# Kernel optimization log

Hardware: AMD Instinct MI355X
Metric: run time of the kernel (lower is better)

The kernel has to match this reference:

```python
import jax, jax.numpy as jnp
import numpy as np

N_NODES = 50000
N_EDGES = 800000
N_GRAPHS = 128
D_IN = 128
D_HID = 128
D_OUT = 3


def setup_inputs() -> dict:
    key = jax.random.key(0)
    ks = jax.random.split(key, 8)

    def lin_w(k, fan_in, fan_out):
        return (jax.random.normal(k, (fan_in, fan_out), jnp.float32)
                * (1.0 / np.sqrt(fan_in)))

    return {
        "x": jax.random.normal(ks[0], (N_NODES, D_IN), jnp.float32),
        "edge_index": jax.random.randint(ks[1], (2, N_EDGES), 0, N_NODES),
        "batch": jnp.sort(jax.random.randint(ks[2], (N_NODES,), 0, N_GRAPHS)),
        "W1": lin_w(ks[3], D_IN, D_HID),  "b1": jnp.zeros((D_HID,), jnp.float32),
        "W2": lin_w(ks[4], D_HID, D_HID), "b2": jnp.zeros((D_HID,), jnp.float32),
        "W3": lin_w(ks[5], D_HID, D_HID), "b3": jnp.zeros((D_HID,), jnp.float32),
        "Wlin": lin_w(ks[6], D_HID, D_OUT), "blin": jnp.zeros((D_OUT,), jnp.float32),
    }


def reference(x, edge_index, batch, W1, b1, W2, b2, W3, b3, Wlin, blin):
    n = x.shape[0]
    # PyG GCNConv: add self-loops, symmetric normalization D^-1/2 A D^-1/2
    loop = jnp.arange(n)
    row = jnp.concatenate([edge_index[0], loop])  # source nodes [E+N]
    col = jnp.concatenate([edge_index[1], loop])  # target nodes [E+N]
    deg = jax.ops.segment_sum(jnp.ones_like(col, dtype=x.dtype), col,
                              num_segments=n)
    dinv = jnp.where(deg > 0, jax.lax.rsqrt(deg), 0.0)
    norm = dinv[row] * dinv[col]  # [E+N]

    def gcn_conv(h, W, b):
        hw = h @ W                              # [N, D] linear (no bias)
        msg = hw[row] * norm[:, None]           # gather + scale [E+N, D]
        return jax.ops.segment_sum(msg, col, num_segments=n) + b

    h = jax.nn.relu(gcn_conv(x, W1, b1))
    h = jax.nn.relu(gcn_conv(h, W2, b2))
    h = gcn_conv(h, W3, b3)

    # global mean pool over graphs (dropout is identity in eval mode)
    sums = jax.ops.segment_sum(h, batch, num_segments=N_GRAPHS)
    counts = jax.ops.segment_sum(jnp.ones((n,), h.dtype), batch,
                                 num_segments=N_GRAPHS)
    pooled = sums / jnp.maximum(counts, 1.0)[:, None]
    return pooled @ Wlin + blin
```

## Files before the change

### kernel.cpp

```cpp
#include <hip/hip_runtime.h>

#define N_NODES 50000
#define N_EDGES 800000
#define N_GRAPHS 128
#define D 128
#define NCHUNK 196

__device__ __forceinline__ void fma4(float4& a, float w, const float4& h) {
    a.x += w * h.x; a.y += w * h.y; a.z += w * h.z; a.w += w * h.w;
}
__device__ __forceinline__ void add4(float4& a, const float4& h) {
    a.x += h.x; a.y += h.y; a.z += h.z; a.w += h.w;
}

__global__ __launch_bounds__(256) void k_count(const int* __restrict__ col,
                                               int* __restrict__ counts) {
    int e = blockIdx.x * 256 + threadIdx.x;
    if (e < N_EDGES) atomicAdd(&counts[col[e]], 1);
}

__global__ __launch_bounds__(256) void k_dinv(const int* __restrict__ counts,
                                              float* __restrict__ dinv) {
    int i = blockIdx.x * 256 + threadIdx.x;
    if (i < N_NODES) dinv[i] = rsqrtf((float)(counts[i] + 1));
}

__global__ __launch_bounds__(256) void k_chunksum(const int* __restrict__ counts,
                                                  int* __restrict__ partials) {
    __shared__ int s[256];
    int i = blockIdx.x * 256 + threadIdx.x;
    s[threadIdx.x] = (i < N_NODES) ? counts[i] : 0;
    __syncthreads();
    for (int off = 128; off > 0; off >>= 1) {
        if (threadIdx.x < off) s[threadIdx.x] += s[threadIdx.x + off];
        __syncthreads();
    }
    if (threadIdx.x == 0) partials[blockIdx.x] = s[0];
}

__global__ __launch_bounds__(256) void k_scanpart(int* __restrict__ partials, int m) {
    __shared__ int s[256];
    int t = threadIdx.x;
    int orig = (t < m) ? partials[t] : 0;
    s[t] = orig;
    __syncthreads();
    for (int off = 1; off < 256; off <<= 1) {
        int v = (t >= off) ? s[t - off] : 0;
        __syncthreads();
        s[t] += v;
        __syncthreads();
    }
    if (t < m) partials[t] = s[t] - orig;
}

__global__ __launch_bounds__(256) void k_scanchunk(const int* __restrict__ counts,
                                                   const int* __restrict__ partials,
                                                   int* __restrict__ row_ptr,
                                                   int* __restrict__ offs) {
    __shared__ int s[256];
    int i = blockIdx.x * 256 + threadIdx.x;
    int t = threadIdx.x;
    int orig = (i < N_NODES) ? counts[i] : 0;
    s[t] = orig;
    __syncthreads();
    for (int off = 1; off < 256; off <<= 1) {
        int v = (t >= off) ? s[t - off] : 0;
        __syncthreads();
        s[t] += v;
        __syncthreads();
    }
    int ex = s[t] - orig + partials[blockIdx.x];
    if (i < N_NODES) { row_ptr[i] = ex; offs[i] = ex; }
    if (i == N_NODES - 1) row_ptr[N_NODES] = ex + orig;
}

__global__ __launch_bounds__(256) void k_fill(const int* __restrict__ row,
                                              const int* __restrict__ col,
                                              int* __restrict__ offs,
                                              int* __restrict__ esrc) {
    int e = blockIdx.x * 256 + threadIdx.x;
    if (e < N_EDGES) {
        int c = col[e];
        int pos = atomicAdd(&offs[c], 1);
        esrc[pos] = row[e];
    }
}

__global__ __launch_bounds__(256, 5) void k_gemm(const float* __restrict__ H,
                                                 const float* __restrict__ W,
                                                 const float* __restrict__ dinv,
                                                 float* __restrict__ out, int n) {
    __shared__ float Ws[128 * 64];
    const int tid = threadIdx.x;
    const int half = blockIdx.x & 1;
    const int row0 = (blockIdx.x >> 1) * 64;
    {
        const float4* W4 = (const float4*)W;
        float4* Ws4 = (float4*)Ws;
#pragma unroll
        for (int i = 0; i < 8; ++i) {
            int idx = i * 256 + tid;
            int k = idx >> 4, c4 = idx & 15;
            Ws4[idx] = W4[k * 32 + half * 16 + c4];
        }
    }
    __syncthreads();
    const int tx = tid & 15;
    const int ty = tid >> 4;
    const float4* H4 = (const float4*)H;
    const float4* Ws4 = (const float4*)Ws;
    const int r0 = row0 + ty * 4;
    const size_t ra = (size_t)min(r0 + 0, n - 1) * 32;
    const size_t rb = (size_t)min(r0 + 1, n - 1) * 32;
    const size_t rc = (size_t)min(r0 + 2, n - 1) * 32;
    const size_t rd = (size_t)min(r0 + 3, n - 1) * 32;
    float4 acc0 = {0,0,0,0}, acc1 = {0,0,0,0}, acc2 = {0,0,0,0}, acc3 = {0,0,0,0};
#pragma unroll 2
    for (int k4 = 0; k4 < 32; ++k4) {
        float4 a0 = H4[ra + k4];
        float4 a1 = H4[rb + k4];
        float4 a2 = H4[rc + k4];
        float4 a3 = H4[rd + k4];
        float4 b0 = Ws4[(k4 * 4 + 0) * 16 + tx];
        float4 b1 = Ws4[(k4 * 4 + 1) * 16 + tx];
        float4 b2 = Ws4[(k4 * 4 + 2) * 16 + tx];
        float4 b3 = Ws4[(k4 * 4 + 3) * 16 + tx];
        fma4(acc0, a0.x, b0); fma4(acc0, a0.y, b1); fma4(acc0, a0.z, b2); fma4(acc0, a0.w, b3);
        fma4(acc1, a1.x, b0); fma4(acc1, a1.y, b1); fma4(acc1, a1.z, b2); fma4(acc1, a1.w, b3);
        fma4(acc2, a2.x, b0); fma4(acc2, a2.y, b1); fma4(acc2, a2.z, b2); fma4(acc2, a2.w, b3);
        fma4(acc3, a3.x, b0); fma4(acc3, a3.y, b1); fma4(acc3, a3.z, b2); fma4(acc3, a3.w, b3);
    }
    float4* o4 = (float4*)out;
    const int co = half * 16 + tx;
    if (r0 + 0 < n) { float d = dinv[r0 + 0]; acc0.x *= d; acc0.y *= d; acc0.z *= d; acc0.w *= d; o4[(size_t)(r0 + 0) * 32 + co] = acc0; }
    if (r0 + 1 < n) { float d = dinv[r0 + 1]; acc1.x *= d; acc1.y *= d; acc1.z *= d; acc1.w *= d; o4[(size_t)(r0 + 1) * 32 + co] = acc1; }
    if (r0 + 2 < n) { float d = dinv[r0 + 2]; acc2.x *= d; acc2.y *= d; acc2.z *= d; acc2.w *= d; o4[(size_t)(r0 + 2) * 32 + co] = acc2; }
    if (r0 + 3 < n) { float d = dinv[r0 + 3]; acc3.x *= d; acc3.y *= d; acc3.z *= d; acc3.w *= d; o4[(size_t)(r0 + 3) * 32 + co] = acc3; }
}

template <int RELU>
__global__ __launch_bounds__(256) void k_agg(const float* __restrict__ Y,
                                             const int* __restrict__ rp,
                                             const int* __restrict__ esrc,
                                             const float* __restrict__ dinv,
                                             const float* __restrict__ bias,
                                             float* __restrict__ out) {
    int wid = (blockIdx.x * 256 + threadIdx.x) >> 6;
    int c = __builtin_amdgcn_readfirstlane(wid);
    if (c >= N_NODES) return;
    const int lane = threadIdx.x & 63;
    const int half = lane >> 5;
    const int l = lane & 31;
    const float4* __restrict__ Y4 = (const float4*)Y;
    const int beg = rp[c], end = rp[c + 1];
    float4 acc0 = {0,0,0,0}, acc1 = {0,0,0,0};
    int jj = beg + half;
    for (; jj + 2 < end; jj += 4) {
        int s0 = esrc[jj];
        int s1 = esrc[jj + 2];
        float4 h0 = Y4[(size_t)s0 * 32 + l];
        float4 h1 = Y4[(size_t)s1 * 32 + l];
        add4(acc0, h0);
        add4(acc1, h1);
    }
    for (; jj < end; jj += 2) add4(acc0, Y4[(size_t)esrc[jj] * 32 + l]);
    if (half == 0) add4(acc0, Y4[(size_t)c * 32 + l]);
    add4(acc0, acc1);
    acc0.x += __shfl_xor(acc0.x, 32);
    acc0.y += __shfl_xor(acc0.y, 32);
    acc0.z += __shfl_xor(acc0.z, 32);
    acc0.w += __shfl_xor(acc0.w, 32);
    if (half == 0) {
        const float dv = dinv[c];
        float4 bb = ((const float4*)bias)[l];
        float4 r;
        r.x = dv * acc0.x + bb.x;
        r.y = dv * acc0.y + bb.y;
        r.z = dv * acc0.z + bb.z;
        r.w = dv * acc0.w + bb.w;
        if (RELU) {
            r.x = fmaxf(r.x, 0.f); r.y = fmaxf(r.y, 0.f);
            r.z = fmaxf(r.z, 0.f); r.w = fmaxf(r.w, 0.f);
        }
        ((float4*)out)[(size_t)c * 32 + l] = r;
    }
}

__global__ __launch_bounds__(64) void k_pool(const float* __restrict__ h,
                                             const int* __restrict__ batch,
                                             float* __restrict__ psum,
                                             float* __restrict__ pcnt) {
    const int l = threadIdx.x;
    const int start = blockIdx.x * 32;
    if (start >= N_NODES) return;
    const int end = min(start + 32, N_NODES);
    const float2* __restrict__ h2 = (const float2*)h;
    float2 acc = {0.f, 0.f};
    float cnt = 0.f;
    int g = batch[start];
    for (int i = start; i < end; ++i) {
        int gi = batch[i];
        if (gi != g) {
            atomicAdd(&psum[g * D + 2 * l], acc.x);
            atomicAdd(&psum[g * D + 2 * l + 1], acc.y);
            if (l == 0) atomicAdd(&pcnt[g], cnt);
            acc.x = 0.f; acc.y = 0.f; cnt = 0.f; g = gi;
        }
        float2 v = h2[(size_t)i * 64 + l];
        acc.x += v.x; acc.y += v.y; cnt += 1.f;
    }
    atomicAdd(&psum[g * D + 2 * l], acc.x);
    atomicAdd(&psum[g * D + 2 * l + 1], acc.y);
    if (l == 0) atomicAdd(&pcnt[g], cnt);
}

__global__ __launch_bounds__(384) void k_final(const float* __restrict__ psum,
                                               const float* __restrict__ pcnt,
                                               const float* __restrict__ Wlin,
                                               const float* __restrict__ blin,
                                               float* __restrict__ out) {
    int t = threadIdx.x;
    if (t >= N_GRAPHS * 3) return;
    int g = t / 3, o = t % 3;
    float c = fmaxf(pcnt[g], 1.f);
    float acc = 0.f;
#pragma unroll 8
    for (int d = 0; d < D; ++d) acc += psum[g * D + d] * Wlin[d * 3 + o];
    out[t] = acc / c + blin[o];
}

extern "C" void kernel_launch(void* const* d_in, const int* in_sizes, int n_in,
                              void* d_out, int out_size, void* d_ws, size_t ws_size,
                              hipStream_t stream) {
    const float* x    = (const float*)d_in[0];
    const int*   row  = (const int*)d_in[1];
    const int*   col  = ((const int*)d_in[1]) + N_EDGES;
    const int*   batch = (const int*)d_in[2];
    const float* W1 = (const float*)d_in[3];  const float* b1 = (const float*)d_in[4];
    const float* W2 = (const float*)d_in[5];  const float* b2 = (const float*)d_in[6];
    const float* W3 = (const float*)d_in[7];  const float* b3 = (const float*)d_in[8];
    const float* Wlin = (const float*)d_in[9]; const float* blin = (const float*)d_in[10];
    float* out = (float*)d_out;

    char* w = (char*)d_ws;
    size_t off = 0;
    auto alloc = [&](size_t bytes) { void* p = w + off; off += (bytes + 255) & ~(size_t)255; return p; };
    float* dinv    = (float*)alloc(N_NODES * 4);
    int*   counts  = (int*)alloc(N_NODES * 4);
    int*   row_ptr = (int*)alloc((N_NODES + 1) * 4);
    int*   offs    = (int*)alloc(N_NODES * 4);
    int*   partials= (int*)alloc(256 * 4);
    int*   esrc    = (int*)alloc((size_t)N_EDGES * 4);
    float* bufA    = (float*)alloc((size_t)N_NODES * D * 4);
    float* bufB    = (float*)alloc((size_t)N_NODES * D * 4);
    float* psum    = (float*)alloc(N_GRAPHS * D * 4);
    float* pcnt    = (float*)alloc(N_GRAPHS * 4);

    hipMemsetAsync(counts, 0, N_NODES * 4, stream);
    hipMemsetAsync(psum, 0, N_GRAPHS * D * 4, stream);
    hipMemsetAsync(pcnt, 0, N_GRAPHS * 4, stream);

    const int EB = (N_EDGES + 255) / 256;
    k_count<<<EB, 256, 0, stream>>>(col, counts);
    k_dinv<<<NCHUNK, 256, 0, stream>>>(counts, dinv);
    k_chunksum<<<NCHUNK, 256, 0, stream>>>(counts, partials);
    k_scanpart<<<1, 256, 0, stream>>>(partials, NCHUNK);
    k_scanchunk<<<NCHUNK, 256, 0, stream>>>(counts, partials, row_ptr, offs);
    k_fill<<<EB, 256, 0, stream>>>(row, col, offs, esrc);

    const int GB = ((N_NODES + 63) / 64) * 2;
    const int AB = (N_NODES * 64 + 255) / 256;
    const int PB = (N_NODES + 31) / 32;

    k_gemm<<<GB, 256, 0, stream>>>(x, W1, dinv, bufA, N_NODES);
    k_agg<1><<<AB, 256, 0, stream>>>(bufA, row_ptr, esrc, dinv, b1, bufB);
    k_gemm<<<GB, 256, 0, stream>>>(bufB, W2, dinv, bufA, N_NODES);
    k_agg<1><<<AB, 256, 0, stream>>>(bufA, row_ptr, esrc, dinv, b2, bufB);
    k_gemm<<<GB, 256, 0, stream>>>(bufB, W3, dinv, bufA, N_NODES);
    k_agg<0><<<AB, 256, 0, stream>>>(bufA, row_ptr, esrc, dinv, b3, bufB);

    k_pool<<<PB, 64, 0, stream>>>(bufB, batch, psum, pcnt);
    k_final<<<1, 384, 0, stream>>>(psum, pcnt, Wlin, blin, out);
}
```

Measured before the change: 479.9 us.

## Split aggregation across feature slices with 16 parallel edge slots per wave

The aggregation kernel now gives each wave one node and one 16-float feature slice, chosen by the low 3 bits of the block index. The 64 lanes cover 16 edges at once with 4 float4 lanes per edge, and the partial sums are combined with a shuffle tree. This exposes more memory-level parallelism per wave for nodes of low degree, which should help hide gather latency. In exchange each edge index is re-read 8 times, the grid grows eightfold, and every gathered row segment is only 64 bytes.

```diff
diff --git a/kernel.cpp b/kernel.cpp
--- a/kernel.cpp
+++ b/kernel.cpp
@@ -145,44 +145,34 @@
                                              const float* __restrict__ dinv,
                                              const float* __restrict__ bias,
                                              float* __restrict__ out) {
-    int wid = (blockIdx.x * 256 + threadIdx.x) >> 6;
-    int c = __builtin_amdgcn_readfirstlane(wid);
-    if (c >= N_NODES) return;
+    const int q4 = (blockIdx.x & 7) << 2;
+    const int c = (blockIdx.x >> 3) * 4 + (threadIdx.x >> 6);
     const int lane = threadIdx.x & 63;
-    const int half = lane >> 5;
-    const int l = lane & 31;
+    const int slot = lane >> 2;
+    const int fl = lane & 3;
     const float4* __restrict__ Y4 = (const float4*)Y;
     const int beg = rp[c], end = rp[c + 1];
-    float4 acc0 = {0,0,0,0}, acc1 = {0,0,0,0};
-    int jj = beg + half;
-    for (; jj + 2 < end; jj += 4) {
-        int s0 = esrc[jj];
-        int s1 = esrc[jj + 2];
-        float4 h0 = Y4[(size_t)s0 * 32 + l];
-        float4 h1 = Y4[(size_t)s1 * 32 + l];
-        add4(acc0, h0);
-        add4(acc1, h1);
-    }
-    for (; jj < end; jj += 2) add4(acc0, Y4[(size_t)esrc[jj] * 32 + l]);
-    if (half == 0) add4(acc0, Y4[(size_t)c * 32 + l]);
-    add4(acc0, acc1);
-    acc0.x += __shfl_xor(acc0.x, 32);
-    acc0.y += __shfl_xor(acc0.y, 32);
-    acc0.z += __shfl_xor(acc0.z, 32);
-    acc0.w += __shfl_xor(acc0.w, 32);
-    if (half == 0) {
+    float4 A = {0,0,0,0};
+    for (int j = beg + slot; j < end; j += 16)
+        add4(A, Y4[(size_t)esrc[j] * 32 + q4 + fl]);
+    A.x += __shfl_xor(A.x, 4);  A.y += __shfl_xor(A.y, 4);  A.z += __shfl_xor(A.z, 4);  A.w += __shfl_xor(A.w, 4);
+    A.x += __shfl_xor(A.x, 8);  A.y += __shfl_xor(A.y, 8);  A.z += __shfl_xor(A.z, 8);  A.w += __shfl_xor(A.w, 8);
+    A.x += __shfl_xor(A.x, 16); A.y += __shfl_xor(A.y, 16); A.z += __shfl_xor(A.z, 16); A.w += __shfl_xor(A.w, 16);
+    A.x += __shfl_xor(A.x, 32); A.y += __shfl_xor(A.y, 32); A.z += __shfl_xor(A.z, 32); A.w += __shfl_xor(A.w, 32);
+    if (slot == 0) {
         const float dv = dinv[c];
-        float4 bb = ((const float4*)bias)[l];
+        float4 yc = Y4[(size_t)c * 32 + q4 + fl];
+        float4 bb = ((const float4*)bias)[q4 + fl];
         float4 r;
-        r.x = dv * acc0.x + bb.x;
-        r.y = dv * acc0.y + bb.y;
-        r.z = dv * acc0.z + bb.z;
-        r.w = dv * acc0.w + bb.w;
+        r.x = dv * (A.x + yc.x) + bb.x;
+        r.y = dv * (A.y + yc.y) + bb.y;
+        r.z = dv * (A.z + yc.z) + bb.z;
+        r.w = dv * (A.w + yc.w) + bb.w;
         if (RELU) {
             r.x = fmaxf(r.x, 0.f); r.y = fmaxf(r.y, 0.f);
             r.z = fmaxf(r.z, 0.f); r.w = fmaxf(r.w, 0.f);
         }
-        ((float4*)out)[(size_t)c * 32 + l] = r;
+        ((float4*)out)[(size_t)c * 32 + q4 + fl] = r;
     }
 }
 
@@ -269,7 +259,7 @@
     k_fill<<<EB, 256, 0, stream>>>(row, col, offs, esrc);
 
     const int GB = ((N_NODES + 63) / 64) * 2;
-    const int AB = (N_NODES * 64 + 255) / 256;
+    const int AB = 8 * (N_NODES / 4);
     const int PB = (N_NODES + 31) / 32;
 
     k_gemm<<<GB, 256, 0, stream>>>(x, W1, dinv, bufA, N_NODES);
```

New measurement: 669.2 us. 39.5% more time.
